# Kernel tuning notes

Hardware: AMD Instinct MI355X
Metric: run time of the kernel (lower is better)

## Reference

```python
import jax, jax.numpy as jnp
import numpy as np

N = 8192        # nodes
E = 49152       # edges (~avg degree 6, triangular mesh)
H = 6           # GATv2 heads
C = 512         # hidden_size (per-head out channels)
F_IN = 2 + C    # GATv2 in_channels = coord(2) + hidden(512)
ALL_FEAT = 37   # deform_in_c-2 + 16 + 16
NUM_LOOP = 3
LRELU_SLOPE = 0.2


def setup_inputs() -> dict:
    key = jax.random.key(0)
    ks = jax.random.split(key, 10)
    x = jax.random.uniform(ks[0], (N, 7), dtype=jnp.float32)
    local_feat = jax.random.normal(ks[1], (N, 16), dtype=jnp.float32)
    conv_feat = jax.random.normal(ks[2], (N, 16), dtype=jnp.float32)
    edge_index = jax.random.randint(ks[3], (2, E), 0, N, dtype=jnp.int64)
    bd_mask = jnp.zeros((N,), jnp.int32)  # poly_mesh=False path
    W_lin = jax.random.normal(ks[4], (ALL_FEAT, C), dtype=jnp.float32) / np.float32(np.sqrt(ALL_FEAT))
    b_lin = jnp.zeros((C,), jnp.float32)
    Wl = jax.random.normal(ks[5], (F_IN, H * C), dtype=jnp.float32) / np.float32(np.sqrt(F_IN))
    Wr = jax.random.normal(ks[6], (F_IN, H * C), dtype=jnp.float32) / np.float32(np.sqrt(F_IN))
    att = jax.random.normal(ks[7], (H, C), dtype=jnp.float32) / np.float32(np.sqrt(C))
    gat_bias = jnp.zeros((C,), jnp.float32)
    W_coord = jax.random.normal(ks[8], (C, 2), dtype=jnp.float32) / np.float32(np.sqrt(C))
    b_coord = jnp.zeros((2,), jnp.float32)
    return dict(x=x, local_feat=local_feat, conv_feat=conv_feat,
                W_lin=W_lin, b_lin=b_lin, Wl=Wl, Wr=Wr, att=att,
                gat_bias=gat_bias, W_coord=W_coord, b_coord=b_coord,
                edge_index=edge_index, bd_mask=bd_mask)


def _gatv2(feat, src, dst, Wl, Wr, att, bias):
    # PyG GATv2Conv: lin_l on source, lin_r on target, additive attention
    n = feat.shape[0]
    xl = (feat @ Wl).reshape(n, H, C)            # source-side transform
    xr = (feat @ Wr).reshape(n, H, C)            # target-side transform
    e = xl[src] + xr[dst]                        # [E', H, C]
    e = jax.nn.leaky_relu(e, LRELU_SLOPE)
    logits = jnp.einsum('ehc,hc->eh', e, att)    # [E', H]
    m = jax.ops.segment_max(logits, dst, num_segments=n)
    m = jnp.where(jnp.isfinite(m), m, 0.0)
    a = jnp.exp(logits - m[dst])
    denom = jax.ops.segment_sum(a, dst, num_segments=n) + 1e-16
    alpha = a / denom[dst]                       # segment softmax over incoming edges
    msg = xl[src] * alpha[:, :, None]            # [E', H, C]
    out = jax.ops.segment_sum(msg, dst, num_segments=n)  # [N, H, C]
    return out.mean(axis=1) + bias               # concat=False -> mean over heads


def reference(x, local_feat, conv_feat, W_lin, b_lin, Wl, Wr, att, gat_bias,
              W_coord, b_coord, edge_index, bd_mask):
    coord = x[:, :2]
    hidden_in = jnp.concatenate([x[:, 2:], local_feat, conv_feat], axis=1)
    hidden = jax.nn.selu(hidden_in @ W_lin + b_lin)
    # GATv2Conv adds self-loops by default
    loops = jnp.arange(N, dtype=edge_index.dtype)
    src = jnp.concatenate([edge_index[0], loops])
    dst = jnp.concatenate([edge_index[1], loops])
    for _ in range(NUM_LOOP):
        up = coord[:, 0] == 1.0
        down = coord[:, 0] == 0.0
        left = coord[:, 1] == 0.0
        right = coord[:, 1] == 1.0
        feat = jnp.concatenate([coord, hidden], axis=1)   # [N, 514]
        hidden = jax.nn.selu(_gatv2(feat, src, dst, Wl, Wr, att, gat_bias))
        out = hidden @ W_coord + b_coord                  # [N, 2]
        ox = jnp.where(down, 0.0, jnp.where(up, 1.0, out[:, 0]))
        oy = jnp.where(right, 1.0, jnp.where(left, 0.0, out[:, 1]))
        coord = jnp.stack([ox, oy], axis=1)
    return coord
```

## Files before the change

kernel.cpp:

```cpp
#include <hip/hip_runtime.h>
#include <hip/hip_bf16.h>
#include <math.h>

#define N_NODES   8192
#define NUM_E     49152
#define NUM_EDGES (NUM_E + N_NODES)
#define H_HEADS   6
#define C_DIM     512
#define HC        (H_HEADS * C_DIM)
#define XLR       (2 * HC)
#define N_FEAT    37
#define LRELU_SLOPE 0.2f
#define SELU_LAMBDA 1.0507009873554805f
#define SELU_ALPHA  1.6732632423543772f

typedef __bf16 bf16_t;
typedef bf16_t bf16x8 __attribute__((ext_vector_type(8)));
typedef float  f32x4  __attribute__((ext_vector_type(4)));
typedef float  f32x2  __attribute__((ext_vector_type(2)));

__device__ __forceinline__ int edge_src(const int* ei, int e) {
    return e < NUM_E ? ei[e] : (e - NUM_E);
}
__device__ __forceinline__ int edge_dst(const int* ei, int e) {
    return e < NUM_E ? ei[NUM_E + e] : (e - NUM_E);
}
__device__ __forceinline__ float selu_f(float v) {
    return v > 0.f ? SELU_LAMBDA * v : SELU_LAMBDA * SELU_ALPHA * (__expf(v) - 1.f);
}
__device__ __forceinline__ void gload_lds16(const void* g, void* l) {
    __builtin_amdgcn_global_load_lds((const __attribute__((address_space(1))) void*)g,
                                     (__attribute__((address_space(3))) void*)l, 16, 0, 0);
}

__global__ __launch_bounds__(512) void k_hidden0(
    const float* __restrict__ x, const float* __restrict__ lf,
    const float* __restrict__ cf, const float* __restrict__ W,
    const float* __restrict__ b, bf16_t* __restrict__ hidden,
    float* __restrict__ coord)
{
    int n = blockIdx.x;
    int c = threadIdx.x;
    __shared__ float f[N_FEAT];
    if (c < 5)            f[c] = x[n*7 + 2 + c];
    else if (c < 21)      f[c] = lf[n*16 + (c-5)];
    else if (c < N_FEAT)  f[c] = cf[n*16 + (c-21)];
    if (c < 2) coord[n*2 + c] = x[n*7 + c];
    __syncthreads();
    float acc = b[c];
    #pragma unroll
    for (int k = 0; k < N_FEAT; ++k) acc = fmaf(f[k], W[k*C_DIM + c], acc);
    hidden[n*C_DIM + c] = (bf16_t)selu_f(acc);
}

__global__ __launch_bounds__(256) void k_wt_transpose(const float* __restrict__ W,
                                                      bf16_t* __restrict__ WT)
{
    __shared__ float tile[32][33];
    int k0 = blockIdx.y * 32;
    int n0 = blockIdx.x * 32;
    int tx = threadIdx.x & 31, ty = threadIdx.x >> 5;
    #pragma unroll
    for (int i = 0; i < 4; ++i)
        tile[ty + i*8][tx] = W[(size_t)(k0 + 2 + ty + i*8) * HC + n0 + tx];
    __syncthreads();
    #pragma unroll
    for (int i = 0; i < 4; ++i)
        WT[(size_t)(n0 + ty + i*8) * C_DIM + k0 + tx] = (bf16_t)tile[tx][ty + i*8];
}

__global__ void k_hist(const int* __restrict__ ei, int* __restrict__ counts) {
    int e = blockIdx.x * blockDim.x + threadIdx.x;
    if (e >= NUM_EDGES) return;
    atomicAdd(&counts[edge_dst(ei, e)], 1);
}

__global__ __launch_bounds__(256) void k_scan(const int* __restrict__ counts,
                                              int* __restrict__ row_ptr,
                                              int* __restrict__ cursor) {
    __shared__ int part[256];
    __shared__ int off[257];
    int t = threadIdx.x;
    int base = t * 32;
    int local[32];
    int s = 0;
    #pragma unroll
    for (int i = 0; i < 32; ++i) { local[i] = s; s += counts[base + i]; }
    part[t] = s;
    __syncthreads();
    if (t == 0) {
        off[0] = 0;
        for (int i = 0; i < 256; ++i) off[i+1] = off[i] + part[i];
    }
    __syncthreads();
    int o = off[t];
    #pragma unroll
    for (int i = 0; i < 32; ++i) {
        int v = o + local[i];
        row_ptr[base + i] = v;
        cursor[base + i]  = v;
    }
    if (t == 255) row_ptr[N_NODES] = off[256];
}

__global__ void k_scatter(const int* __restrict__ ei, int* __restrict__ cursor,
                          int* __restrict__ csr_eid) {
    int e = blockIdx.x * blockDim.x + threadIdx.x;
    if (e >= NUM_EDGES) return;
    int pos = atomicAdd(&cursor[edge_dst(ei, e)], 1);
    csr_eid[pos] = e;
}

#define GM 128
#define GN 128
#define GK 32
__global__ __launch_bounds__(256) void k_gemm_bf16(
    const bf16_t* __restrict__ A,
    const bf16_t* __restrict__ BT,
    const float*  __restrict__ Wl,
    const float*  __restrict__ Wr,
    const float*  __restrict__ coord,
    bf16_t* __restrict__ out)
{
    __shared__ bf16_t As[GM][GK];
    __shared__ bf16_t Bs[GN][GK];
    int tid  = threadIdx.x;
    int wave = tid >> 6;
    int lane = tid & 63;
    int rowBase = blockIdx.y * GM;
    int colBase = blockIdx.x * GN;
    int wr = (wave >> 1) * 64;
    int wc = (wave & 1) * 64;

    f32x4 acc[4][4] = {};

    const bf16_t* Ag = A  + (size_t)(rowBase + wave*32 + (lane >> 2)) * C_DIM + (lane & 3) * 8;
    const bf16_t* Bg = BT + (size_t)(colBase + wave*32 + (lane >> 2)) * C_DIM + (lane & 3) * 8;
    int m16 = lane & 15;
    int q8  = (lane >> 4) * 8;

    for (int k0 = 0; k0 < C_DIM; k0 += GK) {
        gload_lds16(Ag + k0,            &As[wave*32     ][0]);
        gload_lds16(Ag + k0 + 16*C_DIM, &As[wave*32 + 16][0]);
        gload_lds16(Bg + k0,            &Bs[wave*32     ][0]);
        gload_lds16(Bg + k0 + 16*C_DIM, &Bs[wave*32 + 16][0]);
        __syncthreads();
        bf16x8 af[4], bfr[4];
        #pragma unroll
        for (int i = 0; i < 4; ++i) af[i]  = *(const bf16x8*)&As[wr + i*16 + m16][q8];
        #pragma unroll
        for (int j = 0; j < 4; ++j) bfr[j] = *(const bf16x8*)&Bs[wc + j*16 + m16][q8];
        #pragma unroll
        for (int i = 0; i < 4; ++i)
            #pragma unroll
            for (int j = 0; j < 4; ++j)
                acc[i][j] = __builtin_amdgcn_mfma_f32_16x16x32_bf16(af[i], bfr[j], acc[i][j], 0, 0, 0);
        __syncthreads();
    }

    const float* Wtop = (colBase < HC) ? Wl : Wr;
    int coff = (colBase < HC) ? 0 : HC;

    int ccol  = lane & 15;
    int crow4 = (lane >> 4) * 4;
    #pragma unroll
    for (int i = 0; i < 4; ++i) {
        #pragma unroll
        for (int r = 0; r < 4; ++r) {
            int row = rowBase + wr + i*16 + crow4 + r;
            float c0 = coord[row*2 + 0], c1 = coord[row*2 + 1];
            size_t rb = (size_t)row * XLR;
            #pragma unroll
            for (int j = 0; j < 4; ++j) {
                int col = colBase + wc + j*16 + ccol;
                int wcol = col - coff;
                out[rb + col] = (bf16_t)(acc[i][j][r] + c0 * Wtop[wcol] + c1 * Wtop[HC + wcol]);
            }
        }
    }
}

#define MAX_DEG 128
__global__ __launch_bounds__(384) void k_attn_agg(
    const bf16_t* __restrict__ xlr,
    const int* __restrict__ row_ptr, const int* __restrict__ csr_eid,
    const int* __restrict__ ei, const float* __restrict__ att,
    const float* __restrict__ gat_bias, const float* __restrict__ W_coord,
    const float* __restrict__ b_coord, const float* __restrict__ coord_in,
    bf16_t* __restrict__ hidden, float* __restrict__ coord_out)
{
    int n = blockIdx.x;
    int tid = threadIdx.x;
    int h = tid >> 6, lane = tid & 63;
    __shared__ int   s_src[MAX_DEG];
    __shared__ float s_acc[HC];
    __shared__ float s_red[12];

    int beg = row_ptr[n];
    int deg = min(row_ptr[n + 1] - beg, MAX_DEG);
    for (int j = tid; j < deg; j += 384) s_src[j] = edge_src(ei, csr_eid[beg + j]);
    __syncthreads();

    size_t off = (size_t)h * C_DIM + lane * 8;
    bf16x8 xrv = *(const bf16x8*)(xlr + (size_t)n * XLR + HC + off);
    f32x2 xr2[4], at2[4], ac2[4] = {};
    #pragma unroll
    for (int i = 0; i < 4; ++i) {
        xr2[i] = f32x2{(float)xrv[2*i], (float)xrv[2*i+1]};
        at2[i] = f32x2{att[off + 2*i], att[off + 2*i + 1]};
    }

    float l = 0.f;
    bf16x8 xlv = *(const bf16x8*)(xlr + (size_t)s_src[0] * XLR + off);
    for (int j = 0; j < deg; ++j) {
        bf16x8 nxt = xlv;
        if (j + 1 < deg) nxt = *(const bf16x8*)(xlr + (size_t)s_src[j + 1] * XLR + off);
        f32x2 xl2[4];
        #pragma unroll
        for (int i = 0; i < 4; ++i) xl2[i] = f32x2{(float)xlv[2*i], (float)xlv[2*i+1]};
        f32x2 s2 = {0.f, 0.f};
        #pragma unroll
        for (int i = 0; i < 4; ++i) {
            f32x2 v = xl2[i] + xr2[i];
            f32x2 lr = __builtin_elementwise_max(v, v * LRELU_SLOPE);
            s2 += lr * at2[i];
        }
        float sum = s2.x + s2.y;
        #pragma unroll
        for (int o = 1; o < 64; o <<= 1) sum += __shfl_xor(sum, o);
        float a = __expf(sum);
        l += a;
        #pragma unroll
        for (int i = 0; i < 4; ++i) ac2[i] += a * xl2[i];
        xlv = nxt;
    }
    float invl = 1.f / (l + 1e-16f) * (1.f / 6.f);
    #pragma unroll
    for (int i = 0; i < 4; ++i) {
        s_acc[off + 2*i]     = ac2[i].x * invl;
        s_acc[off + 2*i + 1] = ac2[i].y * invl;
    }
    __syncthreads();

    float p0 = 0.f, p1 = 0.f;
    for (int c = tid; c < C_DIM; c += 384) {
        float s = 0.f;
        #pragma unroll
        for (int hh = 0; hh < H_HEADS; ++hh) s += s_acc[hh * C_DIM + c];
        float hv = selu_f(s + gat_bias[c]);
        hidden[n * C_DIM + c] = (bf16_t)hv;
        p0 = fmaf(hv, W_coord[c * 2 + 0], p0);
        p1 = fmaf(hv, W_coord[c * 2 + 1], p1);
    }
    #pragma unroll
    for (int o = 32; o > 0; o >>= 1) { p0 += __shfl_down(p0, o); p1 += __shfl_down(p1, o); }
    if (lane == 0) { s_red[h * 2] = p0; s_red[h * 2 + 1] = p1; }
    __syncthreads();
    if (tid == 0) {
        float o0 = b_coord[0], o1 = b_coord[1];
        #pragma unroll
        for (int w = 0; w < H_HEADS; ++w) { o0 += s_red[w * 2]; o1 += s_red[w * 2 + 1]; }
        float cx = coord_in[n * 2 + 0], cy = coord_in[n * 2 + 1];
        float ox = (cx == 0.0f) ? 0.f : ((cx == 1.0f) ? 1.f : o0);
        float oy = (cy == 1.0f) ? 1.f : ((cy == 0.0f) ? 0.f : o1);
        coord_out[n * 2 + 0] = ox;
        coord_out[n * 2 + 1] = oy;
    }
}

extern "C" void kernel_launch(void* const* d_in, const int* in_sizes, int n_in,
                              void* d_out, int out_size, void* d_ws, size_t ws_size,
                              hipStream_t stream)
{
    const float* x       = (const float*)d_in[0];
    const float* lf      = (const float*)d_in[1];
    const float* cf      = (const float*)d_in[2];
    const float* W_lin   = (const float*)d_in[3];
    const float* b_lin   = (const float*)d_in[4];
    const float* Wl      = (const float*)d_in[5];
    const float* Wr      = (const float*)d_in[6];
    const float* att     = (const float*)d_in[7];
    const float* gbias   = (const float*)d_in[8];
    const float* W_coord = (const float*)d_in[9];
    const float* b_coord = (const float*)d_in[10];
    const int*   ei      = (const int*)d_in[11];

    char* w = (char*)d_ws;
    auto alloc = [&](size_t bytes) { char* p = w; w += (bytes + 255) & ~255ull; return p; };
    bf16_t*   hidden  = (bf16_t*)alloc((size_t)N_NODES * C_DIM * 2);
    bf16_t*   WT      = (bf16_t*)alloc((size_t)XLR * C_DIM * 2);
    bf16_t*   xlr     = (bf16_t*)alloc((size_t)N_NODES * XLR * 2);
    int*      counts  = (int*)alloc((size_t)N_NODES * 4);
    int*      row_ptr = (int*)alloc((size_t)(N_NODES + 1) * 4);
    int*      cursor  = (int*)alloc((size_t)N_NODES * 4);
    int*      csr_eid = (int*)alloc((size_t)NUM_EDGES * 4);
    float*    cA      = (float*)alloc((size_t)N_NODES * 2 * 4);
    float*    cB      = (float*)alloc((size_t)N_NODES * 2 * 4);

    hipMemsetAsync(counts, 0, (size_t)N_NODES * 4, stream);
    k_hidden0<<<N_NODES, 512, 0, stream>>>(x, lf, cf, W_lin, b_lin, hidden, cA);
    {
        dim3 tg(HC / 32, C_DIM / 32);
        k_wt_transpose<<<tg, 256, 0, stream>>>(Wl, WT);
        k_wt_transpose<<<tg, 256, 0, stream>>>(Wr, WT + (size_t)HC * C_DIM);
    }
    k_hist<<<(NUM_EDGES + 255) / 256, 256, 0, stream>>>(ei, counts);
    k_scan<<<1, 256, 0, stream>>>(counts, row_ptr, cursor);
    k_scatter<<<(NUM_EDGES + 255) / 256, 256, 0, stream>>>(ei, cursor, csr_eid);

    float* cin = cA;
    for (int it = 0; it < 3; ++it) {
        float* cout = (it == 2) ? (float*)d_out : ((it == 0) ? cB : cA);
        dim3 g(XLR / GN, N_NODES / GM);
        k_gemm_bf16<<<g, 256, 0, stream>>>(hidden, WT, Wl, Wr, cin, xlr);
        k_attn_agg<<<N_NODES, 384, 0, stream>>>(xlr, row_ptr, csr_eid, ei, att,
                                                gbias, W_coord, b_coord, cin, hidden, cout);
        cin = cout;
    }
}
```

Baseline: 594.7 us.

## Swizzle GEMM LDS tiles and process two edges per attention iteration

The GEMM now XOR-swizzles the k-chunk offset used when loading A and B tiles into LDS and applies the matching swizzle on reads, so fragment loads spread across LDS banks instead of conflicting. Separately, the per-node attention loop handles two neighbour edges per iteration, interleaving their loads, wave reductions and exp calls to expose more instruction-level parallelism. The swizzle has to match on the write and read sides to stay correct. The two-edge loop drops the one-ahead prefetch, which may hurt latency hiding and adds register pressure.

```diff
diff --git a/kernel.cpp b/kernel.cpp
--- a/kernel.cpp
+++ b/kernel.cpp
@@ -134,10 +134,11 @@
 
     f32x4 acc[4][4] = {};
 
-    const bf16_t* Ag = A  + (size_t)(rowBase + wave*32 + (lane >> 2)) * C_DIM + (lane & 3) * 8;
-    const bf16_t* Bg = BT + (size_t)(colBase + wave*32 + (lane >> 2)) * C_DIM + (lane & 3) * 8;
+    int gsw = (((lane & 3) ^ ((lane >> 3) & 3))) * 8;
+    const bf16_t* Ag = A  + (size_t)(rowBase + wave*32 + (lane >> 2)) * C_DIM + gsw;
+    const bf16_t* Bg = BT + (size_t)(colBase + wave*32 + (lane >> 2)) * C_DIM + gsw;
     int m16 = lane & 15;
-    int q8  = (lane >> 4) * 8;
+    int q8s = (((lane >> 4) ^ ((lane >> 1) & 3))) * 8;
 
     for (int k0 = 0; k0 < C_DIM; k0 += GK) {
         gload_lds16(Ag + k0,            &As[wave*32     ][0]);
@@ -147,9 +148,9 @@
         __syncthreads();
         bf16x8 af[4], bfr[4];
         #pragma unroll
-        for (int i = 0; i < 4; ++i) af[i]  = *(const bf16x8*)&As[wr + i*16 + m16][q8];
-        #pragma unroll
-        for (int j = 0; j < 4; ++j) bfr[j] = *(const bf16x8*)&Bs[wc + j*16 + m16][q8];
+        for (int i = 0; i < 4; ++i) af[i]  = *(const bf16x8*)&As[wr + i*16 + m16][q8s];
+        #pragma unroll
+        for (int j = 0; j < 4; ++j) bfr[j] = *(const bf16x8*)&Bs[wc + j*16 + m16][q8s];
         #pragma unroll
         for (int i = 0; i < 4; ++i)
             #pragma unroll
@@ -211,29 +212,55 @@
     }
 
     float l = 0.f;
-    bf16x8 xlv = *(const bf16x8*)(xlr + (size_t)s_src[0] * XLR + off);
-    for (int j = 0; j < deg; ++j) {
-        bf16x8 nxt = xlv;
-        if (j + 1 < deg) nxt = *(const bf16x8*)(xlr + (size_t)s_src[j + 1] * XLR + off);
-        f32x2 xl2[4];
-        #pragma unroll
-        for (int i = 0; i < 4; ++i) xl2[i] = f32x2{(float)xlv[2*i], (float)xlv[2*i+1]};
-        f32x2 s2 = {0.f, 0.f};
+    int j = 0;
+    for (; j + 2 <= deg; j += 2) {
+        bf16x8 xa = *(const bf16x8*)(xlr + (size_t)s_src[j]     * XLR + off);
+        bf16x8 xb = *(const bf16x8*)(xlr + (size_t)s_src[j + 1] * XLR + off);
+        f32x2 xla[4], xlb[4];
         #pragma unroll
         for (int i = 0; i < 4; ++i) {
-            f32x2 v = xl2[i] + xr2[i];
-            f32x2 lr = __builtin_elementwise_max(v, v * LRELU_SLOPE);
-            s2 += lr * at2[i];
-        }
-        float sum = s2.x + s2.y;
-        #pragma unroll
-        for (int o = 1; o < 64; o <<= 1) sum += __shfl_xor(sum, o);
-        float a = __expf(sum);
-        l += a;
-        #pragma unroll
-        for (int i = 0; i < 4; ++i) ac2[i] += a * xl2[i];
-        xlv = nxt;
-    }
+            xla[i] = f32x2{(float)xa[2*i], (float)xa[2*i+1]};
+            xlb[i] = f32x2{(float)xb[2*i], (float)xb[2*i+1]};
+        }
+        f32x2 sa = {0.f, 0.f}, sb = {0.f, 0.f};
+        #pragma unroll
+        for (int i = 0; i < 4; ++i) {
+            f32x2 va = xla[i] + xr2[i];
+            f32x2 vb = xlb[i] + xr2[i];
+            sa += __builtin_elementwise_max(va, va * LRELU_SLOPE) * at2[i];
+            sb += __builtin_elementwise_max(vb, vb * LRELU_SLOPE) * at2[i];
+        }
+        float suma = sa.x + sa.y, sumb = sb.x + sb.y;
+        #pragma unroll
+        for (int o = 1; o < 64; o <<= 1) {
+            suma += __shfl_xor(suma, o);
+            sumb += __shfl_xor(sumb, o);
+        }
+        float aa = __expf(suma), ab = __expf(sumb);
+        l += aa + ab;
+        #pragma unroll
+        for (int i = 0; i < 4; ++i) ac2[i] += aa * xla[i] + ab * xlb[i];
+    }
+    if (j < deg) {
+        bf16x8 xa = *(const bf16x8*)(xlr + (size_t)s_src[j] * XLR + off);
+        f32x2 xla[4];
+        #pragma unroll
+        for (int i = 0; i < 4; ++i) xla[i] = f32x2{(float)xa[2*i], (float)xa[2*i+1]};
+        f32x2 sa = {0.f, 0.f};
+        #pragma unroll
+        for (int i = 0; i < 4; ++i) {
+            f32x2 va = xla[i] + xr2[i];
+            sa += __builtin_elementwise_max(va, va * LRELU_SLOPE) * at2[i];
+        }
+        float suma = sa.x + sa.y;
+        #pragma unroll
+        for (int o = 1; o < 64; o <<= 1) suma += __shfl_xor(suma, o);
+        float aa = __expf(suma);
+        l += aa;
+        #pragma unroll
+        for (int i = 0; i < 4; ++i) ac2[i] += aa * xla[i];
+    }
+
     float invl = 1.f / (l + 1e-16f) * (1.f / 6.f);
     #pragma unroll
     for (int i = 0; i < 4; ++i) {
```

Result: no change. 590.7 us (-0.7%).
